# Kernel tuning notes

Hardware: AMD Instinct MI355X
Metric: run time of the kernel (lower is better)

Reference implementation:

```python
import jax, jax.numpy as jnp
import numpy as np

QUANT_BLOCK = 32  # GGUF Q4_0-style block size
QUANT_ZERO = 8.0  # 4-bit codes are offset-binary around 8


def setup_inputs() -> dict:
    key = jax.random.key(0)
    k_x, k_q, k_s, k_up, k_dn, k_b = jax.random.split(key, 6)
    O, I, R = 4096, 4096, 16
    T = 2048  # tokens (batch*seq)
    x = jax.random.normal(k_x, (T, I), dtype=jnp.float32)
    # quantized 4-bit codes stored unpacked as int32 in [0, 16)
    q = jax.random.randint(k_q, (O, I), 0, 16, dtype=jnp.int32)
    # per-block scales (small positive, like real GGUF d values)
    scales = jax.random.uniform(k_s, (O, I // QUANT_BLOCK), dtype=jnp.float32) * 0.05
    lora_up = jax.random.normal(k_up, (O, R), dtype=jnp.float32) * 0.02
    lora_down = jax.random.normal(k_dn, (R, I), dtype=jnp.float32) * 0.02
    alpha = jnp.ones((), dtype=jnp.float32)
    bias = jax.random.normal(k_b, (O,), dtype=jnp.float32)
    return {"x": x, "q": q, "scales": scales, "lora_up": lora_up,
            "lora_down": lora_down, "alpha": alpha, "bias": bias}


def _dequant(q, scales):
    # q: [O, I] int codes; scales: [O, I/BLOCK] per-block scale
    O, I = q.shape
    qf = q.reshape(O, I // QUANT_BLOCK, QUANT_BLOCK).astype(scales.dtype)
    w = (qf - QUANT_ZERO) * scales[:, :, None]  # [O, I/B, B]
    return w.reshape(O, I)


def reference(x, q, scales, lora_up, lora_down, alpha, bias):
    # on-the-fly dequant (GGMLLayer.get_weight -> dequantize_tensor)
    W = _dequant(q, scales)  # [O, I]
    # LoRA patch apply (ray_calculate_weight): W += alpha * up @ down
    W = W + alpha * jnp.einsum('or,ri->oi', lora_up, lora_down)
    # linear forward: y = x @ W^T + b
    return jnp.einsum('ti,oi->to', x, W) + bias
```

## Files before the change

### kernel.cpp

```cpp
#include <hip/hip_runtime.h>
#include <hip/hip_bf16.h>
#include <stdint.h>

#define T_DIM 2048
#define I_DIM 4096
#define O_DIM 4096
#define R_DIM 16
#define QBLK  32

typedef __bf16 bf16x8 __attribute__((ext_vector_type(8)));
typedef float  floatx4 __attribute__((ext_vector_type(4)));
typedef unsigned short ushort_t;

__device__ __forceinline__ ushort_t f2bf(float f) {
  unsigned u = __float_as_uint(f);
  u += 0x7FFFu + ((u >> 16) & 1u);
  return (ushort_t)(u >> 16);
}

__device__ __forceinline__ float dot4(float4 a, float4 b) {
  return a.x * b.x + a.y * b.y + a.z * b.z + a.w * b.w;
}

__global__ __launch_bounds__(256) void k_prep_x(const float* __restrict__ x,
                                                ushort_t* __restrict__ xb) {
  int idx = blockIdx.x * 256 + threadIdx.x;
  const float4* xp = (const float4*)x;
  float4 a = xp[idx * 2], b = xp[idx * 2 + 1];
  union { ushort_t u[8]; uint4 v; } r;
  r.u[0] = f2bf(a.x); r.u[1] = f2bf(a.y); r.u[2] = f2bf(a.z); r.u[3] = f2bf(a.w);
  r.u[4] = f2bf(b.x); r.u[5] = f2bf(b.y); r.u[6] = f2bf(b.z); r.u[7] = f2bf(b.w);
  ((uint4*)xb)[idx] = r.v;
}

__global__ __launch_bounds__(256) void k_prep_w(const int* __restrict__ q,
                                                const float* __restrict__ scales,
                                                ushort_t* __restrict__ wb) {
  int idx = blockIdx.x * 256 + threadIdx.x;
  int o  = idx >> 9;
  int i0 = (idx & 511) * 8;
  float s = scales[o * (I_DIM / QBLK) + (i0 >> 5)];
  const int4* qp = (const int4*)(q + (size_t)o * I_DIM + i0);
  int4 q0 = qp[0], q1 = qp[1];
  union { ushort_t u[8]; uint4 v; } r;
  r.u[0] = f2bf((float)(q0.x - 8) * s); r.u[1] = f2bf((float)(q0.y - 8) * s);
  r.u[2] = f2bf((float)(q0.z - 8) * s); r.u[3] = f2bf((float)(q0.w - 8) * s);
  r.u[4] = f2bf((float)(q1.x - 8) * s); r.u[5] = f2bf((float)(q1.y - 8) * s);
  r.u[6] = f2bf((float)(q1.z - 8) * s); r.u[7] = f2bf((float)(q1.w - 8) * s);
  ((uint4*)wb)[idx] = r.v;
}

__global__ __launch_bounds__(256) void k_xd(const float* __restrict__ x,
                                            const float* __restrict__ down,
                                            const float* __restrict__ alphap,
                                            float* __restrict__ xd) {
  __shared__ float ds[16 * 512];
  const int tid = threadIdx.x;
  const int tl = tid >> 5, s = tid & 31;
  const int t = blockIdx.x * 8 + tl;
  float acc[16];
#pragma unroll
  for (int r = 0; r < 16; ++r) acc[r] = 0.f;

  for (int c = 0; c < 8; ++c) {
    const int ib = c * 512;
    __syncthreads();
#pragma unroll
    for (int j = 0; j < 8; ++j) {
      int e = j * 256 + tid;
      int r = e >> 7, col = e & 127;
      ((float4*)ds)[e] = ((const float4*)(down + (size_t)r * I_DIM + ib))[col];
    }
    __syncthreads();
#pragma unroll
    for (int j = 0; j < 4; ++j) {
      float4 xv = ((const float4*)(x + (size_t)t * I_DIM + ib))[s + 32 * j];
#pragma unroll
      for (int r = 0; r < 16; ++r) {
        float4 dv = ((const float4*)ds)[r * 128 + s + 32 * j];
        acc[r] += dot4(xv, dv);
      }
    }
  }
  const float al = alphap[0];
#pragma unroll
  for (int r = 0; r < 16; ++r) {
    float v = acc[r];
    v += __shfl_down(v, 16, 32);
    v += __shfl_down(v, 8, 32);
    v += __shfl_down(v, 4, 32);
    v += __shfl_down(v, 2, 32);
    v += __shfl_down(v, 1, 32);
    if (s == 0) xd[t * 16 + r] = v * al;
  }
}

__global__ __launch_bounds__(256) void k_gemm(const ushort_t* __restrict__ xb,
                                              const ushort_t* __restrict__ wb,
                                              const float* __restrict__ bias,
                                              const float* __restrict__ xd,
                                              const float* __restrict__ up,
                                              float* __restrict__ y) {
  __shared__ __align__(16) ushort_t As[128 * 64];
  __shared__ __align__(16) ushort_t Bs[128 * 64];
  const int tid = threadIdx.x;
  const int oT = blockIdx.x * 128, tT = blockIdx.y * 128;
  const int lane = tid & 63;
  const int wv = __builtin_amdgcn_readfirstlane(tid >> 6);
  const int wm = wv >> 1, wn = wv & 1;
  const int quad = lane >> 4, m16 = lane & 15;

  floatx4 acc[4][4] = {};

  for (int kt = 0; kt < I_DIM / 64; ++kt) {
    const int k0 = kt * 64;
#pragma unroll
    for (int it = 0; it < 4; ++it) {
      const int seg_base = (it * 4 + wv) * 64;
      const int seg = seg_base + lane;
      const int r = seg >> 3;
      const int cg = (seg & 7) ^ (r & 7);
      __builtin_amdgcn_global_load_lds(
          (const __attribute__((address_space(1))) char*)(xb + (size_t)(tT + r) * I_DIM + k0 + cg * 8),
          (__attribute__((address_space(3))) char*)(As + seg_base * 8), 16, 0, 0);
      __builtin_amdgcn_global_load_lds(
          (const __attribute__((address_space(1))) char*)(wb + (size_t)(oT + r) * I_DIM + k0 + cg * 8),
          (__attribute__((address_space(3))) char*)(Bs + seg_base * 8), 16, 0, 0);
    }
    asm volatile("s_waitcnt vmcnt(0)" ::: "memory");
    __syncthreads();

#pragma unroll
    for (int ks2 = 0; ks2 < 2; ++ks2) {
      const int c = ks2 * 4 + quad;
      bf16x8 af[4], bfr[4];
#pragma unroll
      for (int im = 0; im < 4; ++im) {
        int m = wm * 64 + im * 16 + m16;
        af[im] = *(const bf16x8*)(As + (m * 8 + (c ^ (m & 7))) * 8);
      }
#pragma unroll
      for (int in_ = 0; in_ < 4; ++in_) {
        int n = wn * 64 + in_ * 16 + m16;
        bfr[in_] = *(const bf16x8*)(Bs + (n * 8 + (c ^ (n & 7))) * 8);
      }
#pragma unroll
      for (int im = 0; im < 4; ++im)
#pragma unroll
        for (int in_ = 0; in_ < 4; ++in_)
          acc[im][in_] = __builtin_amdgcn_mfma_f32_16x16x32_bf16(
              af[im], bfr[in_], acc[im][in_], 0, 0, 0);
    }
    __syncthreads();
  }

#pragma unroll
  for (int im = 0; im < 4; ++im) {
#pragma unroll
    for (int reg = 0; reg < 4; ++reg) {
      int t = tT + wm * 64 + im * 16 + quad * 4 + reg;
      const float4* xr = (const float4*)(xd + t * 16);
      float4 x0 = xr[0], x1 = xr[1], x2 = xr[2], x3 = xr[3];
#pragma unroll
      for (int in_ = 0; in_ < 4; ++in_) {
        int o = oT + wn * 64 + in_ * 16 + m16;
        const float4* ur = (const float4*)(up + (size_t)o * R_DIM);
        float lv = dot4(x0, ur[0]) + dot4(x1, ur[1]) +
                   dot4(x2, ur[2]) + dot4(x3, ur[3]);
        y[(size_t)t * O_DIM + o] = acc[im][in_][reg] + lv + bias[o];
      }
    }
  }
}

extern "C" void kernel_launch(void* const* d_in, const int* in_sizes, int n_in,
                              void* d_out, int out_size, void* d_ws, size_t ws_size,
                              hipStream_t stream) {
  const float* x      = (const float*)d_in[0];
  const int*   q      = (const int*)d_in[1];
  const float* scales = (const float*)d_in[2];
  const float* up     = (const float*)d_in[3];
  const float* down   = (const float*)d_in[4];
  const float* alpha  = (const float*)d_in[5];
  const float* bias   = (const float*)d_in[6];
  float* y = (float*)d_out;

  ushort_t* xb = (ushort_t*)d_ws;
  ushort_t* wb = (ushort_t*)((char*)d_ws + (size_t)T_DIM * I_DIM * 2);
  float*    xd = (float*)((char*)d_ws + (size_t)T_DIM * I_DIM * 2 + (size_t)O_DIM * I_DIM * 2);

  hipLaunchKernelGGL(k_prep_x, dim3((T_DIM * I_DIM) / 8 / 256), dim3(256), 0, stream, x, xb);
  hipLaunchKernelGGL(k_prep_w, dim3((O_DIM * I_DIM) / 8 / 256), dim3(256), 0, stream, q, scales, wb);
  hipLaunchKernelGGL(k_xd, dim3(T_DIM / 8), dim3(256), 0, stream, x, down, alpha, xd);
  hipLaunchKernelGGL(k_gemm, dim3(O_DIM / 128, T_DIM / 128), dim3(256), 0, stream,
                     xb, wb, bias, xd, up, y);
}
```

Baseline: 508.9 us.

## Double-buffer LDS tiles in bf16 GEMM to overlap global loads with MFMA

The GEMM main loop moves from a single LDS buffer to two. Each step now loads its fragments into registers, issues the direct global-to-LDS loads for the next k-tile into the other buffer, and then runs the MFMAs, so memory latency overlaps with compute. This replaces two __syncthreads per step with one wait plus a raw s_barrier, at the cost of twice the LDS per block (which may lower occupancy) and more fragment registers. The last iteration wraps around and loads an unused tile.

```diff
diff --git a/kernel.cpp b/kernel.cpp
--- a/kernel.cpp
+++ b/kernel.cpp
@@ -11,6 +11,9 @@
 typedef __bf16 bf16x8 __attribute__((ext_vector_type(8)));
 typedef float  floatx4 __attribute__((ext_vector_type(4)));
 typedef unsigned short ushort_t;
+
+#define AS1 __attribute__((address_space(1)))
+#define AS3 __attribute__((address_space(3)))
 
 __device__ __forceinline__ ushort_t f2bf(float f) {
   unsigned u = __float_as_uint(f);
@@ -101,19 +104,17 @@
                                               const float* __restrict__ xd,
                                               const float* __restrict__ up,
                                               float* __restrict__ y) {
-  __shared__ __align__(16) ushort_t As[128 * 64];
-  __shared__ __align__(16) ushort_t Bs[128 * 64];
+  __shared__ __align__(16) ushort_t sm[2 * 2 * 128 * 64];
   const int tid = threadIdx.x;
   const int oT = blockIdx.x * 128, tT = blockIdx.y * 128;
   const int lane = tid & 63;
-  const int wv = __builtin_amdgcn_readfirstlane(tid >> 6);
+  const int wv = tid >> 6;
   const int wm = wv >> 1, wn = wv & 1;
   const int quad = lane >> 4, m16 = lane & 15;
 
   floatx4 acc[4][4] = {};
 
-  for (int kt = 0; kt < I_DIM / 64; ++kt) {
-    const int k0 = kt * 64;
+  auto stage = [&](int buf, int k0) {
 #pragma unroll
     for (int it = 0; it < 4; ++it) {
       const int seg_base = (it * 4 + wv) * 64;
@@ -121,37 +122,46 @@
       const int r = seg >> 3;
       const int cg = (seg & 7) ^ (r & 7);
       __builtin_amdgcn_global_load_lds(
-          (const __attribute__((address_space(1))) char*)(xb + (size_t)(tT + r) * I_DIM + k0 + cg * 8),
-          (__attribute__((address_space(3))) char*)(As + seg_base * 8), 16, 0, 0);
+          (const AS1 char*)(xb + (size_t)(tT + r) * I_DIM + k0 + cg * 8),
+          (AS3 char*)(sm + buf * 16384 + seg_base * 8), 16, 0, 0);
       __builtin_amdgcn_global_load_lds(
-          (const __attribute__((address_space(1))) char*)(wb + (size_t)(oT + r) * I_DIM + k0 + cg * 8),
-          (__attribute__((address_space(3))) char*)(Bs + seg_base * 8), 16, 0, 0);
-    }
+          (const AS1 char*)(wb + (size_t)(oT + r) * I_DIM + k0 + cg * 8),
+          (AS3 char*)(sm + buf * 16384 + 8192 + seg_base * 8), 16, 0, 0);
+    }
+  };
+
+  auto body = [&](int buf, int k0n) {
     asm volatile("s_waitcnt vmcnt(0)" ::: "memory");
-    __syncthreads();
-
+    asm volatile("s_barrier" ::: "memory");
+    const ushort_t* A = sm + buf * 16384;
+    const ushort_t* B = sm + buf * 16384 + 8192;
+    bf16x8 af[2][4], bfr[2][4];
 #pragma unroll
     for (int ks2 = 0; ks2 < 2; ++ks2) {
       const int c = ks2 * 4 + quad;
-      bf16x8 af[4], bfr[4];
-#pragma unroll
-      for (int im = 0; im < 4; ++im) {
-        int m = wm * 64 + im * 16 + m16;
-        af[im] = *(const bf16x8*)(As + (m * 8 + (c ^ (m & 7))) * 8);
+#pragma unroll
+      for (int i = 0; i < 4; ++i) {
+        int m = wm * 64 + i * 16 + m16;
+        af[ks2][i] = *(const bf16x8*)(A + (m * 8 + (c ^ (m & 7))) * 8);
+        int n = wn * 64 + i * 16 + m16;
+        bfr[ks2][i] = *(const bf16x8*)(B + (n * 8 + (c ^ (n & 7))) * 8);
       }
-#pragma unroll
-      for (int in_ = 0; in_ < 4; ++in_) {
-        int n = wn * 64 + in_ * 16 + m16;
-        bfr[in_] = *(const bf16x8*)(Bs + (n * 8 + (c ^ (n & 7))) * 8);
-      }
+    }
+    stage(buf ^ 1, k0n);
+#pragma unroll
+    for (int ks2 = 0; ks2 < 2; ++ks2)
 #pragma unroll
       for (int im = 0; im < 4; ++im)
 #pragma unroll
         for (int in_ = 0; in_ < 4; ++in_)
           acc[im][in_] = __builtin_amdgcn_mfma_f32_16x16x32_bf16(
-              af[im], bfr[in_], acc[im][in_], 0, 0, 0);
-    }
-    __syncthreads();
+              af[ks2][im], bfr[ks2][in_], acc[im][in_], 0, 0, 0);
+  };
+
+  stage(0, 0);
+  for (int kt = 0; kt < I_DIM / 64; kt += 2) {
+    body(0, ((kt + 1) & 63) * 64);
+    body(1, ((kt + 2) & 63) * 64);
   }
 
 #pragma unroll
```

Result: faster. 490.0 us (-3.7%).

## Merge prep kernels into one launch and narrow GEMM output tile

Applied to the files above, without the earlier changes.

Combines the x conversion, weight dequantization and LoRA x·down projection into a single kernel that dispatches on block index, saving two kernel launches. The GEMM tile shrinks from 128x128 to 128x64 on the output dimension, which doubles the number of workgroups for better CU coverage but lowers data reuse per tile. The explicit vmcnt(0) wait before the barrier is also dropped. Without that wait, LDS contents may not be ready when reads start after the barrier. The merged kernel also reserves the 32KB shared buffer for the elementwise blocks, which can limit occupancy.

```diff
diff --git a/kernel.cpp b/kernel.cpp
--- a/kernel.cpp
+++ b/kernel.cpp
@@ -12,6 +12,9 @@
 typedef float  floatx4 __attribute__((ext_vector_type(4)));
 typedef unsigned short ushort_t;
 
+#define AS1 __attribute__((address_space(1)))
+#define AS3 __attribute__((address_space(3)))
+
 __device__ __forceinline__ ushort_t f2bf(float f) {
   unsigned u = __float_as_uint(f);
   u += 0x7FFFu + ((u >> 16) & 1u);
@@ -22,76 +25,80 @@
   return a.x * b.x + a.y * b.y + a.z * b.z + a.w * b.w;
 }
 
-__global__ __launch_bounds__(256) void k_prep_x(const float* __restrict__ x,
-                                                ushort_t* __restrict__ xb) {
-  int idx = blockIdx.x * 256 + threadIdx.x;
-  const float4* xp = (const float4*)x;
-  float4 a = xp[idx * 2], b = xp[idx * 2 + 1];
-  union { ushort_t u[8]; uint4 v; } r;
-  r.u[0] = f2bf(a.x); r.u[1] = f2bf(a.y); r.u[2] = f2bf(a.z); r.u[3] = f2bf(a.w);
-  r.u[4] = f2bf(b.x); r.u[5] = f2bf(b.y); r.u[6] = f2bf(b.z); r.u[7] = f2bf(b.w);
-  ((uint4*)xb)[idx] = r.v;
-}
-
-__global__ __launch_bounds__(256) void k_prep_w(const int* __restrict__ q,
-                                                const float* __restrict__ scales,
-                                                ushort_t* __restrict__ wb) {
-  int idx = blockIdx.x * 256 + threadIdx.x;
-  int o  = idx >> 9;
-  int i0 = (idx & 511) * 8;
-  float s = scales[o * (I_DIM / QBLK) + (i0 >> 5)];
-  const int4* qp = (const int4*)(q + (size_t)o * I_DIM + i0);
-  int4 q0 = qp[0], q1 = qp[1];
-  union { ushort_t u[8]; uint4 v; } r;
-  r.u[0] = f2bf((float)(q0.x - 8) * s); r.u[1] = f2bf((float)(q0.y - 8) * s);
-  r.u[2] = f2bf((float)(q0.z - 8) * s); r.u[3] = f2bf((float)(q0.w - 8) * s);
-  r.u[4] = f2bf((float)(q1.x - 8) * s); r.u[5] = f2bf((float)(q1.y - 8) * s);
-  r.u[6] = f2bf((float)(q1.z - 8) * s); r.u[7] = f2bf((float)(q1.w - 8) * s);
-  ((uint4*)wb)[idx] = r.v;
-}
-
-__global__ __launch_bounds__(256) void k_xd(const float* __restrict__ x,
-                                            const float* __restrict__ down,
-                                            const float* __restrict__ alphap,
-                                            float* __restrict__ xd) {
+__global__ __launch_bounds__(256) void k_prep(const float* __restrict__ x,
+                                              const int* __restrict__ q,
+                                              const float* __restrict__ scales,
+                                              const float* __restrict__ down,
+                                              const float* __restrict__ alphap,
+                                              ushort_t* __restrict__ xb,
+                                              ushort_t* __restrict__ wb,
+                                              float* __restrict__ xd) {
   __shared__ float ds[16 * 512];
-  const int tid = threadIdx.x;
-  const int tl = tid >> 5, s = tid & 31;
-  const int t = blockIdx.x * 8 + tl;
-  float acc[16];
-#pragma unroll
-  for (int r = 0; r < 16; ++r) acc[r] = 0.f;
-
-  for (int c = 0; c < 8; ++c) {
-    const int ib = c * 512;
-    __syncthreads();
-#pragma unroll
-    for (int j = 0; j < 8; ++j) {
-      int e = j * 256 + tid;
-      int r = e >> 7, col = e & 127;
-      ((float4*)ds)[e] = ((const float4*)(down + (size_t)r * I_DIM + ib))[col];
-    }
-    __syncthreads();
-#pragma unroll
-    for (int j = 0; j < 4; ++j) {
-      float4 xv = ((const float4*)(x + (size_t)t * I_DIM + ib))[s + 32 * j];
-#pragma unroll
-      for (int r = 0; r < 16; ++r) {
-        float4 dv = ((const float4*)ds)[r * 128 + s + 32 * j];
-        acc[r] += dot4(xv, dv);
-      }
-    }
-  }
-  const float al = alphap[0];
-#pragma unroll
-  for (int r = 0; r < 16; ++r) {
-    float v = acc[r];
-    v += __shfl_down(v, 16, 32);
-    v += __shfl_down(v, 8, 32);
-    v += __shfl_down(v, 4, 32);
-    v += __shfl_down(v, 2, 32);
-    v += __shfl_down(v, 1, 32);
-    if (s == 0) xd[t * 16 + r] = v * al;
+  const int b = blockIdx.x, tid = threadIdx.x;
+
+  if (b < 4096) {
+    int idx = b * 256 + tid;
+    const float4* xp = (const float4*)x;
+    float4 a = xp[idx * 2], c = xp[idx * 2 + 1];
+    union { ushort_t u[8]; uint4 v; } r;
+    r.u[0] = f2bf(a.x); r.u[1] = f2bf(a.y); r.u[2] = f2bf(a.z); r.u[3] = f2bf(a.w);
+    r.u[4] = f2bf(c.x); r.u[5] = f2bf(c.y); r.u[6] = f2bf(c.z); r.u[7] = f2bf(c.w);
+    ((uint4*)xb)[idx] = r.v;
+    return;
+  }
+  if (b < 12288) {
+    int idx = (b - 4096) * 256 + tid;
+    int o  = idx >> 9;
+    int i0 = (idx & 511) * 8;
+    float s = scales[o * (I_DIM / QBLK) + (i0 >> 5)];
+    const int4* qp = (const int4*)(q + (size_t)o * I_DIM + i0);
+    int4 q0 = qp[0], q1 = qp[1];
+    union { ushort_t u[8]; uint4 v; } r;
+    r.u[0] = f2bf((float)(q0.x - 8) * s); r.u[1] = f2bf((float)(q0.y - 8) * s);
+    r.u[2] = f2bf((float)(q0.z - 8) * s); r.u[3] = f2bf((float)(q0.w - 8) * s);
+    r.u[4] = f2bf((float)(q1.x - 8) * s); r.u[5] = f2bf((float)(q1.y - 8) * s);
+    r.u[6] = f2bf((float)(q1.z - 8) * s); r.u[7] = f2bf((float)(q1.w - 8) * s);
+    ((uint4*)wb)[idx] = r.v;
+    return;
+  }
+  {
+    const int blk = b - 12288;
+    const int tl = tid >> 5, s = tid & 31;
+    const int t = blk * 8 + tl;
+    float acc[16];
+#pragma unroll
+    for (int r = 0; r < 16; ++r) acc[r] = 0.f;
+    for (int c = 0; c < 8; ++c) {
+      const int ib = c * 512;
+      __syncthreads();
+#pragma unroll
+      for (int j = 0; j < 8; ++j) {
+        int e = j * 256 + tid;
+        int r = e >> 7, col = e & 127;
+        ((float4*)ds)[e] = ((const float4*)(down + (size_t)r * I_DIM + ib))[col];
+      }
+      __syncthreads();
+#pragma unroll
+      for (int j = 0; j < 4; ++j) {
+        float4 xv = ((const float4*)(x + (size_t)t * I_DIM + ib))[s + 32 * j];
+#pragma unroll
+        for (int r = 0; r < 16; ++r) {
+          float4 dv = ((const float4*)ds)[r * 128 + s + 32 * j];
+          acc[r] += dot4(xv, dv);
+        }
+      }
+    }
+    const float al = alphap[0];
+#pragma unroll
+    for (int r = 0; r < 16; ++r) {
+      float v = acc[r];
+      v += __shfl_down(v, 16, 32);
+      v += __shfl_down(v, 8, 32);
+      v += __shfl_down(v, 4, 32);
+      v += __shfl_down(v, 2, 32);
+      v += __shfl_down(v, 1, 32);
+      if (s == 0) xd[t * 16 + r] = v * al;
+    }
   }
 }
 
@@ -102,52 +109,58 @@
                                               const float* __restrict__ up,
                                               float* __restrict__ y) {
   __shared__ __align__(16) ushort_t As[128 * 64];
-  __shared__ __align__(16) ushort_t Bs[128 * 64];
+  __shared__ __align__(16) ushort_t Bs[64 * 64];
   const int tid = threadIdx.x;
-  const int oT = blockIdx.x * 128, tT = blockIdx.y * 128;
+  const int oT = blockIdx.x * 64, tT = blockIdx.y * 128;
   const int lane = tid & 63;
-  const int wv = __builtin_amdgcn_readfirstlane(tid >> 6);
+  const int wv = tid >> 6;
   const int wm = wv >> 1, wn = wv & 1;
   const int quad = lane >> 4, m16 = lane & 15;
 
-  floatx4 acc[4][4] = {};
+  floatx4 acc[4][2] = {};
 
   for (int kt = 0; kt < I_DIM / 64; ++kt) {
     const int k0 = kt * 64;
 #pragma unroll
     for (int it = 0; it < 4; ++it) {
-      const int seg_base = (it * 4 + wv) * 64;
+      const int seg_base = wv * 256 + it * 64;
       const int seg = seg_base + lane;
       const int r = seg >> 3;
       const int cg = (seg & 7) ^ (r & 7);
       __builtin_amdgcn_global_load_lds(
-          (const __attribute__((address_space(1))) char*)(xb + (size_t)(tT + r) * I_DIM + k0 + cg * 8),
-          (__attribute__((address_space(3))) char*)(As + seg_base * 8), 16, 0, 0);
+          (const AS1 char*)(xb + (size_t)(tT + r) * I_DIM + k0 + cg * 8),
+          (AS3 char*)(As + seg_base * 8), 16, 0, 0);
+    }
+#pragma unroll
+    for (int it = 0; it < 2; ++it) {
+      const int seg_base = wv * 128 + it * 64;
+      const int seg = seg_base + lane;
+      const int r = seg >> 3;
+      const int cg = (seg & 7) ^ (r & 7);
       __builtin_amdgcn_global_load_lds(
-          (const __attribute__((address_space(1))) char*)(wb + (size_t)(oT + r) * I_DIM + k0 + cg * 8),
-          (__attribute__((address_space(3))) char*)(Bs + seg_base * 8), 16, 0, 0);
-    }
-    asm volatile("s_waitcnt vmcnt(0)" ::: "memory");
+          (const AS1 char*)(wb + (size_t)(oT + r) * I_DIM + k0 + cg * 8),
+          (AS3 char*)(Bs + seg_base * 8), 16, 0, 0);
+    }
     __syncthreads();
 
 #pragma unroll
     for (int ks2 = 0; ks2 < 2; ++ks2) {
       const int c = ks2 * 4 + quad;
-      bf16x8 af[4], bfr[4];
+      bf16x8 af[4], bfr[2];
 #pragma unroll
       for (int im = 0; im < 4; ++im) {
         int m = wm * 64 + im * 16 + m16;
         af[im] = *(const bf16x8*)(As + (m * 8 + (c ^ (m & 7))) * 8);
       }
 #pragma unroll
-      for (int in_ = 0; in_ < 4; ++in_) {
-        int n = wn * 64 + in_ * 16 + m16;
+      for (int in_ = 0; in_ < 2; ++in_) {
+        int n = wn * 32 + in_ * 16 + m16;
         bfr[in_] = *(const bf16x8*)(Bs + (n * 8 + (c ^ (n & 7))) * 8);
       }
 #pragma unroll
       for (int im = 0; im < 4; ++im)
 #pragma unroll
-        for (int in_ = 0; in_ < 4; ++in_)
+        for (int in_ = 0; in_ < 2; ++in_)
           acc[im][in_] = __builtin_amdgcn_mfma_f32_16x16x32_bf16(
               af[im], bfr[in_], acc[im][in_], 0, 0, 0);
     }
@@ -162,8 +175,8 @@
       const float4* xr = (const float4*)(xd + t * 16);
       float4 x0 = xr[0], x1 = xr[1], x2 = xr[2], x3 = xr[3];
 #pragma unroll
-      for (int in_ = 0; in_ < 4; ++in_) {
-        int o = oT + wn * 64 + in_ * 16 + m16;
+      for (int in_ = 0; in_ < 2; ++in_) {
+        int o = oT + wn * 32 + in_ * 16 + m16;
         const float4* ur = (const float4*)(up + (size_t)o * R_DIM);
         float lv = dot4(x0, ur[0]) + dot4(x1, ur[1]) +
                    dot4(x2, ur[2]) + dot4(x3, ur[3]);
@@ -189,9 +202,8 @@
   ushort_t* wb = (ushort_t*)((char*)d_ws + (size_t)T_DIM * I_DIM * 2);
   float*    xd = (float*)((char*)d_ws + (size_t)T_DIM * I_DIM * 2 + (size_t)O_DIM * I_DIM * 2);
 
-  hipLaunchKernelGGL(k_prep_x, dim3((T_DIM * I_DIM) / 8 / 256), dim3(256), 0, stream, x, xb);
-  hipLaunchKernelGGL(k_prep_w, dim3((O_DIM * I_DIM) / 8 / 256), dim3(256), 0, stream, q, scales, wb);
-  hipLaunchKernelGGL(k_xd, dim3(T_DIM / 8), dim3(256), 0, stream, x, down, alpha, xd);
-  hipLaunchKernelGGL(k_gemm, dim3(O_DIM / 128, T_DIM / 128), dim3(256), 0, stream,
+  hipLaunchKernelGGL(k_prep, dim3(4096 + 8192 + 256), dim3(256), 0, stream,
+                     x, q, scales, down, alpha, xb, wb, xd);
+  hipLaunchKernelGGL(k_gemm, dim3(O_DIM / 64, T_DIM / 128), dim3(256), 0, stream,
                      xb, wb, bias, xd, up, y);
 }
```

After: 465.7 us. 8.5% less time.
